# Performance work log

Measured on AMD Instinct MI355X. Metric: run time of the kernel, lower is better.

Reference implementation:

```python
import jax, jax.numpy as jnp
import numpy as np

D_MODEL = 512
DQ = D_MODEL // 4  # 128
TIME_SHIFT_START = 256
VELOCITY_START = 768
NOTE_OFF_START = 128


def conv1d(x, w, b, stride, pad):
    # x: [B, Cin, L], w: [Cout, Cin, K]
    y = jax.lax.conv_general_dilated(x, w, (stride,), [(pad, pad)],
                                     dimension_numbers=('NCH', 'OIH', 'NCH'))
    return y + b[None, :, None]


def adaptive_avg_pool1d(x, out_size):
    # faithful to torch AdaptiveAvgPool1d bin boundaries
    L = x.shape[-1]
    starts = (np.arange(out_size) * L) // out_size
    ends = np.ceil((np.arange(out_size) + 1) * L / out_size).astype(np.int64)
    cs = jnp.concatenate([jnp.zeros(x.shape[:-1] + (1,), x.dtype),
                          jnp.cumsum(x, axis=-1)], axis=-1)
    return (cs[..., ends] - cs[..., starts]) / jnp.asarray(ends - starts, x.dtype)


def setup_inputs() -> dict:
    key = jax.random.key(0)
    ks = jax.random.split(key, 20)

    def w(k, shape):
        fan_in = int(np.prod(shape[1:]))
        return jax.random.normal(k, shape, jnp.float32) / np.sqrt(fan_in)

    def b(k, n):
        return jax.random.normal(k, (n,), jnp.float32) * 0.01

    return {
        'tokens': jax.random.randint(ks[0], (32, 4096), 0, 774),
        'r1_w': w(ks[1], (32, 1, 8)),    'r1_b': b(ks[2], 32),
        'r2_w': w(ks[3], (64, 32, 4)),   'r2_b': b(ks[4], 64),
        'h1_w': w(ks[5], (64, 128, 12)), 'h1_b': b(ks[6], 64),
        'h2_w': w(ks[7], (32, 64, 8)),   'h2_b': b(ks[8], 32),
        'm1_w': w(ks[9], (64, 128, 5)),  'm1_b': b(ks[10], 64),
        'm2_w': w(ks[11], (32, 64, 3)),  'm2_b': b(ks[12], 32),
        'd1_w': w(ks[13], (16, 6, 4)),   'd1_b': b(ks[14], 16),
        'd2_w': w(ks[15], (16, 16, 3)),  'd2_b': b(ks[16], 16),
        'fc_w': w(ks[17], (D_MODEL, D_MODEL)), 'fc_b': b(ks[18], D_MODEL),
    }


def reference(tokens, r1_w, r1_b, r2_w, r2_b, h1_w, h1_b, h2_w, h2_b,
              m1_w, m1_b, m2_w, m2_b, d1_w, d1_b, d2_w, d2_b, fc_w, fc_b):
    B, S = tokens.shape
    relu = jax.nn.relu

    # rhythm: binary time-shift indicator [B,1,S]
    ts = ((tokens >= TIME_SHIFT_START) & (tokens < VELOCITY_START)).astype(jnp.float32)[:, None, :]
    r = relu(conv1d(ts, r1_w, r1_b, 2, 3))
    r = relu(conv1d(r, r2_w, r2_b, 2, 1))
    r = adaptive_avg_pool1d(r, DQ).reshape(B, -1)  # [B, 64*DQ]

    # vectorized one-hot pitch scatter (replaces the python double loop): [B,128,S]
    nm = tokens < NOTE_OFF_START
    pitch = jnp.transpose(
        jax.nn.one_hot(jnp.where(nm, tokens, 0) % 128, 128, dtype=jnp.float32)
        * nm[..., None].astype(jnp.float32), (0, 2, 1))

    h = relu(conv1d(pitch, h1_w, h1_b, 1, 6))
    h = relu(conv1d(h, h2_w, h2_b, 2, 3))
    h = adaptive_avg_pool1d(h, DQ).reshape(B, -1)  # [B, 32*DQ]

    m = relu(conv1d(pitch, m1_w, m1_b, 1, 2))
    m = relu(conv1d(m, m2_w, m2_b, 1, 1))
    m = adaptive_avg_pool1d(m, DQ).reshape(B, -1)  # [B, 32*DQ]

    # velocity one-hot scatter: [B,6,S]
    vm = tokens >= VELOCITY_START
    vel = jnp.clip(jnp.where(vm, tokens - VELOCITY_START, 0), 0, 5)
    vpat = jnp.transpose(
        jax.nn.one_hot(vel, 6, dtype=jnp.float32) * vm[..., None].astype(jnp.float32),
        (0, 2, 1))
    d = relu(conv1d(vpat, d1_w, d1_b, 1, 2))
    d = relu(conv1d(d, d2_w, d2_b, 1, 1))
    d = adaptive_avg_pool1d(d, DQ).reshape(B, -1)  # [B, 16*DQ]

    # total flattened size is 36*d_model != d_model, so torch branch always pools
    r, h, m, d = [adaptive_avg_pool1d(f[:, None, :], DQ)[:, 0] for f in (r, h, m, d)]

    combined = jnp.concatenate([r, h, m, d], axis=1)       # [B, d_model]
    feats = combined @ fc_w.T + fc_b                        # Linear
    return jnp.broadcast_to(feats[:, None, :], (B, S, D_MODEL))
```

## Files before the change

kernel.cpp:

```cpp
#include <hip/hip_runtime.h>

typedef unsigned short u16;
typedef unsigned int u32;
typedef float vf4 __attribute__((ext_vector_type(4)));
typedef unsigned int vu4 __attribute__((ext_vector_type(4)));
typedef short sh8 __attribute__((ext_vector_type(8)));
typedef float f32x4 __attribute__((ext_vector_type(4)));

__device__ __forceinline__ float bf2f(u16 u) {
  return __uint_as_float(((u32)u) << 16);
}
__device__ __forceinline__ u16 f2bf(float f) {
  u32 x = __float_as_uint(f);
  return (u16)((x + 0x7fffu + ((x >> 16) & 1u)) >> 16);
}
__device__ __forceinline__ float ldin(const void* p, int idx, int isf) {
  return isf ? ((const float*)p)[idx] : bf2f(((const u16*)p)[idx]);
}

#define OFF_FLAG  ((size_t)0)
#define OFF_WB    ((size_t)16)
#define OFF_WTH1  ((size_t)1180432)
#define OFF_WTM1  ((size_t)1573648)
#define OFF_COMB  ((size_t)1737488)
#define OFF_FEATF ((size_t)1803024)
#define OFF_FEATB ((size_t)1868560)
#define OFF_R1    ((size_t)1901328)
#define OFF_D1    ((size_t)10289936)
#define OFF_DP    ((size_t)18686736)
#define OFF_H1    ((size_t)18948880)
#define OFF_M1    ((size_t)35758864)
#define OFF_WH2B  ((size_t)52536080)
#define OFF_WH2L  ((size_t)52568848)
#define OFF_WM2B  ((size_t)52601616)
#define OFF_WM2L  ((size_t)52613904)
#define WS_NEEDED ((size_t)52626192)

#define WB_R1W 0
#define WB_R1B 256
#define WB_R2W 288
#define WB_R2B 8480
#define WB_H1B 8544
#define WB_H2W 8608
#define WB_H2B 24992
#define WB_M1B 25024
#define WB_M2W 25088
#define WB_M2B 31232
#define WB_D1W 31264
#define WB_D1B 31648
#define WB_D2W 31664
#define WB_D2B 32432
#define WB_FCW 32448
#define WB_FCB 294592
#define WB_TOTAL 295104

#define H1_STRIDE 4104
#define D1_STRIDE 4100

__global__ __launch_bounds__(256) void k_convert(
    const void* r1_w, const void* r1_b, const void* r2_w, const void* r2_b,
    const void* h1_w, const void* h1_b, const void* h2_w, const void* h2_b,
    const void* m1_w, const void* m1_b, const void* m2_w, const void* m2_b,
    const void* d1_w, const void* d1_b, const void* d2_w, const void* d2_b,
    const void* fc_w, const void* fc_b,
    int* __restrict__ flagp, float* __restrict__ wb,
    float* __restrict__ wTh1, float* __restrict__ wTm1,
    float* __restrict__ combined,
    u16* __restrict__ wh2b, u16* __restrict__ wh2l,
    u16* __restrict__ wm2b, u16* __restrict__ wm2l) {
  __shared__ int cnt[4];
  int tid = threadIdx.x;
  {
    u16 v = ((const u16*)fc_w)[2 * tid];
    int e = (v >> 7) & 0xFF;
    int outside = (e < 100 || e > 140) ? 1 : 0;
    unsigned long long m = __ballot(outside);
    if ((tid & 63) == 0) cnt[tid >> 6] = __popcll(m);
  }
  __syncthreads();
  int isf = (cnt[0] + cnt[1] + cnt[2] + cnt[3] >= 64) ? 1 : 0;
  if (blockIdx.x == 0 && tid == 0) flagp[0] = isf;

  int j = blockIdx.x * 256 + tid;
  if (j >= 473280) return;
  if (j < WB_TOTAL) {
    const void* src; int si;
    if      (j < WB_R1B) { src = r1_w; si = j; }
    else if (j < WB_R2W) { src = r1_b; si = j - WB_R1B; }
    else if (j < WB_R2B) { src = r2_w; si = j - WB_R2W; }
    else if (j < WB_H1B) { src = r2_b; si = j - WB_R2B; }
    else if (j < WB_H2W) { src = h1_b; si = j - WB_H1B; }
    else if (j < WB_H2B) { src = h2_w; si = j - WB_H2W; }
    else if (j < WB_M1B) { src = h2_b; si = j - WB_H2B; }
    else if (j < WB_M2W) { src = m1_b; si = j - WB_M1B; }
    else if (j < WB_M2B) { src = m2_w; si = j - WB_M2W; }
    else if (j < WB_D1W) { src = m2_b; si = j - WB_M2B; }
    else if (j < WB_D1B) { src = d1_w; si = j - WB_D1W; }
    else if (j < WB_D2W) { src = d1_b; si = j - WB_D1B; }
    else if (j < WB_D2B) { src = d2_w; si = j - WB_D2W; }
    else if (j < WB_FCW) { src = d2_b; si = j - WB_D2B; }
    else if (j < WB_FCB) { src = fc_w; si = j - WB_FCW; }
    else                 { src = fc_b; si = j - WB_FCB; }
    wb[j] = ldin(src, si, isf);
  } else if (j < 393408) {
    int j2 = j - WB_TOTAL;
    int o = j2 & 63, r = j2 >> 6, k = r % 12, p = r / 12;
    wTh1[j2] = ldin(h1_w, (o * 128 + p) * 12 + k, isf);
  } else if (j < 434368) {
    int j3 = j - 393408;
    int o = j3 & 63, r = j3 >> 6, k = r % 5, p = r / 5;
    wTm1[j3] = ldin(m1_w, (o * 128 + p) * 5 + k, isf);
  } else if (j < 450752) {
    combined[j - 434368] = 0.f;
  } else if (j < 467136) {
    int jj = j - 450752;
    int o = jj >> 9, rem = jj & 511, c = rem >> 3, kk = rem & 7;
    float w = ldin(h2_w, (o * 64 + c) * 8 + kk, isf);
    u16 hi = f2bf(w);
    wh2b[jj] = hi;
    wh2l[jj] = f2bf(w - bf2f(hi));
  } else {
    int jj = j - 467136;
    int o = jj / 192, rem = jj % 192, c = rem / 3, kk = rem % 3;
    float w = ldin(m2_w, (o * 64 + c) * 3 + kk, isf);
    u16 hi = f2bf(w);
    wm2b[jj] = hi;
    wm2l[jj] = f2bf(w - bf2f(hi));
  }
}


__device__ __forceinline__ void dev_r1(float* smem, const int* tok,
                                       const float* r1wf, const float* r1bf,
                                       float* r1ws, int chunk, int b) {
  float* w1s = smem;
  float* b1s = smem + 256;
  float* Ibuf = smem + 288;
  int tid = threadIdx.x;
  w1s[tid] = r1wf[tid];
  if (tid < 32) b1s[tid] = r1bf[tid];
  int t0 = chunk * 64;
  if (tid < 134) {
    int x = 2 * t0 - 3 + tid;
    float v = 0.f;
    if ((unsigned)x < 4096u) {
      int tk = tok[b * 4096 + x];
      v = (tk >= 256 && tk < 768) ? 1.f : 0.f;
    }
    Ibuf[tid] = v;
  }
  __syncthreads();
  int tl = tid & 63, og = tid >> 6;
  float iv[8];
#pragma unroll
  for (int k = 0; k < 8; ++k) iv[k] = Ibuf[2 * tl + k];
  int t = t0 + tl;
#pragma unroll
  for (int i = 0; i < 8; ++i) {
    int o = og * 8 + i;
    float acc = b1s[o];
#pragma unroll
    for (int k = 0; k < 8; ++k) acc = fmaf(w1s[o * 8 + k], iv[k], acc);
    r1ws[(size_t)(b * 32 + o) * 2048 + t] = fmaxf(acc, 0.f);
  }
}

__device__ __forceinline__ void dev_d1(float* smem, const int* tok,
                                       const float* d1wf, const float* d1bf,
                                       float* d1ws, int chunk, int b) {
  float* wds = smem;
  int* cls = (int*)(smem + 384);
  int tid = threadIdx.x;
  for (int f = tid; f < 384; f += 256) wds[f] = d1wf[f];
  int t0 = chunk * 64;
  if (tid < 67) {
    int x = t0 - 2 + tid;
    int v = -1;
    if ((unsigned)x < 4096u) {
      int tk = tok[b * 4096 + x];
      if (tk >= 768) { v = tk - 768; v = v > 5 ? 5 : v; }
    }
    cls[tid] = v;
  }
  __syncthreads();
  int tl = tid & 63, og = tid >> 6;
  int t = t0 + tl;
  if (t > 4096) return;
  int vk[4];
#pragma unroll
  for (int k = 0; k < 4; ++k) vk[k] = cls[tl + k];
#pragma unroll
  for (int i = 0; i < 4; ++i) {
    int o = og * 4 + i;
    float acc = d1bf[o];
#pragma unroll
    for (int k = 0; k < 4; ++k) {
      int v = vk[k];
      if (v >= 0) acc += wds[(o * 6 + v) * 4 + k];
    }
    d1ws[(size_t)(b * 16 + o) * D1_STRIDE + t] = fmaxf(acc, 0.f);
  }
}

__device__ __forceinline__ void dev_h1(float* smem, const int* tok,
                                       const float* wTh1, const float* h1bf,
                                       u16* h1ws, int bx, int b) {
  float (*tile)[65] = reinterpret_cast<float(*)[65]>(smem);
  int tid = threadIdx.x;
  int t0 = bx * 32;
  int o = tid & 63, sub = tid >> 6;
  float bias = h1bf[o];
#pragma unroll
  for (int j = 0; j < 8; ++j) {
    int tl = j * 4 + sub;
    int t = t0 + tl;
    float acc = bias;
    if (t <= 4096) {
#pragma unroll
      for (int k = 0; k < 12; ++k) {
        int x = t + k - 6;
        if ((unsigned)x < 4096u) {
          int p = tok[b * 4096 + x];
          if (p < 128) acc += wTh1[(p * 12 + k) * 64 + o];
        }
      }
    }
    tile[tl][o] = fmaxf(acc, 0.f);
  }
  __syncthreads();
  int o2 = tid >> 2, seg = tid & 3;
  size_t rowbase = (size_t)(b * 64 + o2) * H1_STRIDE;
  int ts = t0 + seg * 8;
  if (ts + 7 <= 4096) {
    u32 w0 = (u32)f2bf(tile[seg * 8 + 0][o2]) | ((u32)f2bf(tile[seg * 8 + 1][o2]) << 16);
    u32 w1 = (u32)f2bf(tile[seg * 8 + 2][o2]) | ((u32)f2bf(tile[seg * 8 + 3][o2]) << 16);
    u32 w2 = (u32)f2bf(tile[seg * 8 + 4][o2]) | ((u32)f2bf(tile[seg * 8 + 5][o2]) << 16);
    u32 w3 = (u32)f2bf(tile[seg * 8 + 6][o2]) | ((u32)f2bf(tile[seg * 8 + 7][o2]) << 16);
    uint4 v; v.x = w0; v.y = w1; v.z = w2; v.w = w3;
    *(uint4*)&h1ws[rowbase + ts] = v;
  } else {
    for (int i2 = 0; i2 < 8; ++i2) {
      int t = ts + i2;
      if (t <= 4096) h1ws[rowbase + t] = f2bf(tile[seg * 8 + i2][o2]);
      else if (t < H1_STRIDE) h1ws[rowbase + t] = 0;
    }
  }
}

__device__ __forceinline__ void dev_m1(float* smem, const int* tok,
                                       const float* wTm1, const float* m1bf,
                                       u16* m1ws, int bx, int b) {
  float (*tile)[65] = reinterpret_cast<float(*)[65]>(smem);
  int tid = threadIdx.x;
  int t0 = bx * 32;
  int o = tid & 63, sub = tid >> 6;
  float bias = m1bf[o];
#pragma unroll
  for (int j = 0; j < 8; ++j) {
    int tl = j * 4 + sub;
    int t = t0 + tl;
    float acc = bias;
#pragma unroll
    for (int k = 0; k < 5; ++k) {
      int x = t + k - 2;
      if ((unsigned)x < 4096u) {
        int p = tok[b * 4096 + x];
        if (p < 128) acc += wTm1[(p * 5 + k) * 64 + o];
      }
    }
    tile[tl][o] = fmaxf(acc, 0.f);
  }
  __syncthreads();
  int o2 = tid >> 2, seg = tid & 3;
  size_t rowbase = (size_t)(b * 64 + o2) * 4096;
  int ts = t0 + seg * 8;
  u32 w0 = (u32)f2bf(tile[seg * 8 + 0][o2]) | ((u32)f2bf(tile[seg * 8 + 1][o2]) << 16);
  u32 w1 = (u32)f2bf(tile[seg * 8 + 2][o2]) | ((u32)f2bf(tile[seg * 8 + 3][o2]) << 16);
  u32 w2 = (u32)f2bf(tile[seg * 8 + 4][o2]) | ((u32)f2bf(tile[seg * 8 + 5][o2]) << 16);
  u32 w3 = (u32)f2bf(tile[seg * 8 + 6][o2]) | ((u32)f2bf(tile[seg * 8 + 7][o2]) << 16);
  uint4 v; v.x = w0; v.y = w1; v.z = w2; v.w = w3;
  *(uint4*)&m1ws[rowbase + ts] = v;
}

__global__ __launch_bounds__(256) void k_cv1(const int* __restrict__ tok,
                                             const float* __restrict__ wb,
                                             const float* __restrict__ wTh1,
                                             const float* __restrict__ wTm1,
                                             float* __restrict__ r1ws,
                                             float* __restrict__ d1ws,
                                             u16* __restrict__ h1ws,
                                             u16* __restrict__ m1ws) {
  __shared__ __align__(16) float smem[2080];
  int bx = blockIdx.x;
  if (bx < 1024) {
    dev_r1(smem, tok, wb + WB_R1W, wb + WB_R1B, r1ws, bx & 31, bx >> 5);
  } else if (bx < 3104) {
    int n = bx - 1024;
    dev_d1(smem, tok, wb + WB_D1W, wb + WB_D1B, d1ws, n % 65, n / 65);
  } else if (bx < 7232) {
    int n = bx - 3104;
    dev_h1(smem, tok, wTh1, wb + WB_H1B, h1ws, n % 129, n / 129);
  } else {
    int n = bx - 7232;
    dev_m1(smem, tok, wTm1, wb + WB_M1B, m1ws, n & 127, n >> 7);
  }
}


__device__ __forceinline__ void dev_h2(const u16* h1ws,
                                       const u16* wh2b, const u16* wh2l,
                                       const float* h2bf,
                                       float* combined, int chunk, int q, int b) {
  const int tid = threadIdx.x;
  const int w = tid >> 6, l = tid & 63;
  const int quad = l >> 4, n = l & 15;
  const int ot = w & 1, tp = w >> 1;
  const int tb = q * 512 + chunk * 64;
  f32x4 acc[2];
  acc[0] = (f32x4){0.f, 0.f, 0.f, 0.f};
  acc[1] = (f32x4){0.f, 0.f, 0.f, 0.f};
  const u16* wph = wh2b + (size_t)(16 * ot + n) * 512 + quad * 8;
  const u16* wpl = wh2l + (size_t)(16 * ot + n) * 512 + quad * 8;

  for (int kc = 0; kc < 2; ++kc) {
    sh8 ah[8], al[8];
#pragma unroll
    for (int s = 0; s < 8; ++s) {
      ah[s] = *(const sh8*)(wph + kc * 256 + 32 * s);
      al[s] = *(const sh8*)(wpl + kc * 256 + 32 * s);
    }
#pragma unroll
    for (int it = 0; it < 2; ++it) {
      int t0 = tb + (2 * it + tp) * 16;
      int xbase = 2 * t0 + 2 * n - 3;
#pragma unroll
      for (int s = 0; s < 8; ++s) {
        int c = kc * 32 + 4 * s + quad;
        const u16* row = h1ws + (size_t)(b * 64 + c) * H1_STRIDE;
        sh8 bb;
        if (xbase >= 0) {
          __builtin_memcpy(&bb, row + xbase, 16);
        } else {
#pragma unroll
          for (int j = 0; j < 8; ++j) {
            int x = xbase + j;
            bb[j] = (x >= 0) ? (short)row[x] : (short)0;
          }
        }
        acc[it] = __builtin_amdgcn_mfma_f32_16x16x32_bf16(ah[s], bb, acc[it], 0, 0, 0);
        acc[it] = __builtin_amdgcn_mfma_f32_16x16x32_bf16(al[s], bb, acc[it], 0, 0, 0);
      }
    }
  }
#pragma unroll
  for (int r = 0; r < 4; ++r) {
    float bs = h2bf[16 * ot + quad * 4 + r];
    float s = fmaxf(acc[0][r] + bs, 0.f) + fmaxf(acc[1][r] + bs, 0.f);
    s += __shfl_xor(s, 1, 64);
    s += __shfl_xor(s, 2, 64);
    s += __shfl_xor(s, 4, 64);
    s += __shfl_xor(s, 8, 64);
    if (n == 0) {
      int o = 16 * ot + quad * 4 + r;
      atomicAdd(&combined[b * 512 + 128 + 4 * o + q], s * (1.f / 512.f));
    }
  }
}

__device__ __forceinline__ void dev_m2(float* smem, const u16* m1ws,
                                       const u16* wm2b, const u16* wm2l,
                                       const float* m2bf,
                                       float* combined, int sub, int q, int b) {
  u16* xs = (u16*)smem;
  const int tid = threadIdx.x;
  const int w = tid >> 6, l = tid & 63;
  const int quad = l >> 4, n = l & 15;
  const int ot = w & 1, tp = w >> 1;
  const int tb = q * 1024 + sub * 256;
  sh8 ah[6], al[6];
  {
    const u16* wph = wm2b + (size_t)(16 * ot + n) * 192 + quad * 8;
    const u16* wpl = wm2l + (size_t)(16 * ot + n) * 192 + quad * 8;
#pragma unroll
    for (int s = 0; s < 6; ++s) {
      ah[s] = *(const sh8*)(wph + 32 * s);
      al[s] = *(const sh8*)(wpl + 32 * s);
    }
  }
  float bs[4];
#pragma unroll
  for (int r = 0; r < 4; ++r) bs[r] = m2bf[16 * ot + quad * 4 + r];
  float sm[4] = {0.f, 0.f, 0.f, 0.f};
  const int gkb = quad * 8;

  for (int it = 0; it < 8; ++it) {
    for (int f = tid; f < 1280; f += 256) {
      int rg = f / 640, rem = f % 640, c = rem / 10, ch = rem % 10;
      int t0 = tb + (2 * it + rg) * 16;
      int xa = t0 - 2 + 2 * ch;
      const u16* row = m1ws + (size_t)(b * 64 + c) * 4096;
      u32 vlo = ((unsigned)xa < 4096u) ? row[xa] : 0u;
      u32 vhi = ((unsigned)(xa + 1) < 4096u) ? row[xa + 1] : 0u;
      ((u32*)xs)[f] = vlo | (vhi << 16);
    }
    __syncthreads();
    const u16* xr = xs + tp * 1280;
    f32x4 acc = {0.f, 0.f, 0.f, 0.f};
#pragma unroll
    for (int s = 0; s < 6; ++s) {
      sh8 bb;
#pragma unroll
      for (int j = 0; j < 8; ++j) {
        int gk = 32 * s + gkb + j;
        int c = (gk * 21846) >> 16;
        int kk = gk - 3 * c;
        bb[j] = (short)xr[c * 20 + n + kk + 1];
      }
      acc = __builtin_amdgcn_mfma_f32_16x16x32_bf16(ah[s], bb, acc, 0, 0, 0);
      acc = __builtin_amdgcn_mfma_f32_16x16x32_bf16(al[s], bb, acc, 0, 0, 0);
    }
#pragma unroll
    for (int r = 0; r < 4; ++r) sm[r] += fmaxf(acc[r] + bs[r], 0.f);
    __syncthreads();
  }
#pragma unroll
  for (int r = 0; r < 4; ++r) {
    float s = sm[r];
    s += __shfl_xor(s, 1, 64);
    s += __shfl_xor(s, 2, 64);
    s += __shfl_xor(s, 4, 64);
    s += __shfl_xor(s, 8, 64);
    if (n == 0) {
      int o = 16 * ot + quad * 4 + r;
      atomicAdd(&combined[b * 512 + 256 + 4 * o + q], s * (1.f / 1024.f));
    }
  }
}

__device__ __forceinline__ void dev_r2(float* smem, const float* r1ws,
                                       const float* r2wf, const float* r2bf,
                                       float* combined, int chunk, int b) {
  float* wcr = smem;
  float (*tile)[68] = reinterpret_cast<float(*)[68]>(smem + 2048);
  const int tbase = chunk * 64;
  const int half = chunk >> 3;
  const int tid = threadIdx.x;
  const int og = tid >> 6, tl = tid & 63;
  float acc[16];
#pragma unroll
  for (int i = 0; i < 16; ++i) acc[i] = 0.f;

  for (int c0 = 0; c0 < 32; c0 += 8) {
    for (int f = tid; f < 2048; f += 256) {
      int o = f & 63, r = f >> 6, k = r & 3, cc = r >> 2;
      wcr[f] = r2wf[(o * 32 + c0 + cc) * 4 + k];
    }
    for (int f = tid; f < 1056; f += 256) {
      int iu = f % 66, pc = f / 66, p = pc & 1, cc = pc >> 1;
      int x = 2 * (tbase - 1 + iu) + p;
      float v = 0.f;
      if (x >= 0 && x < 2048) v = r1ws[(size_t)(b * 32 + c0 + cc) * 2048 + x];
      tile[pc][iu] = v;
    }
    __syncthreads();
#pragma unroll
    for (int cc = 0; cc < 8; ++cc) {
      float ev[3], od[3];
#pragma unroll
      for (int f3 = 0; f3 < 3; ++f3) {
        ev[f3] = tile[cc * 2][tl + f3];
        od[f3] = tile[cc * 2 + 1][tl + f3];
      }
#pragma unroll
      for (int k = 0; k < 4; ++k) {
        const int p = (k + 1) & 1, fk = (k + 1) >> 1;
        const float* wv = &wcr[(cc * 4 + k) * 64 + og * 16];
        float4 wa = *(const float4*)wv;
        float4 wbv = *(const float4*)(wv + 4);
        float4 wcc = *(const float4*)(wv + 8);
        float4 wd = *(const float4*)(wv + 12);
        float wr[16] = {wa.x, wa.y, wa.z, wa.w, wbv.x, wbv.y, wbv.z, wbv.w,
                        wcc.x, wcc.y, wcc.z, wcc.w, wd.x, wd.y, wd.z, wd.w};
        float v0 = p ? od[fk] : ev[fk];
#pragma unroll
        for (int i = 0; i < 16; ++i) acc[i] = fmaf(v0, wr[i], acc[i]);
      }
    }
    __syncthreads();
  }
  const float inv = 1.f / 512.f;
#pragma unroll
  for (int i = 0; i < 16; ++i) {
    int o = og * 16 + i;
    float s = fmaxf(acc[i] + r2bf[o], 0.f);
#pragma unroll
    for (int d = 32; d > 0; d >>= 1) s += __shfl_down(s, d, 64);
    if (tl == 0) atomicAdd(&combined[b * 512 + 2 * o + half], s * inv);
  }
}

__device__ __forceinline__ void dev_d2(float* smem, const float* d1ws,
                                       const float* d2wf, const float* d2bf,
                                       float* dpws, int chunk, int b) {
  float* wd = smem;
  float (*dt)[132] = reinterpret_cast<float(*)[132]>(smem + 768);
  float* c2 = smem + 768 + 2112;
  const int tbase = chunk * 128;
  const int tid = threadIdx.x;
  for (int f = tid; f < 768; f += 256) wd[f] = d2wf[f];
  for (int f = tid; f < 2096; f += 256) {
    int iu = f % 131, c = f / 131;
    int x = tbase - 1 + iu;
    float v = 0.f;
    if (x >= 0 && x <= 4096) v = d1ws[(size_t)(b * 16 + c) * D1_STRIDE + x];
    dt[c][iu] = v;
  }
  __syncthreads();
  for (int idx = tid; idx < 16 * 129; idx += 256) {
    int o = idx / 129, tl = idx % 129;
    float acc = d2bf[o];
    const float* w = &wd[o * 48];
#pragma unroll 4
    for (int c = 0; c < 16; ++c) {
      acc = fmaf(dt[c][tl], w[c * 3 + 0],
            fmaf(dt[c][tl + 1], w[c * 3 + 1],
            fmaf(dt[c][tl + 2], w[c * 3 + 2], acc)));
    }
    c2[o * 133 + tl] = fmaxf(acc, 0.f);
  }
  __syncthreads();
  if (tid < 64) {
    int o = tid >> 2, qq = tid & 3;
    const float* row = c2 + o * 133 + 32 * qq;
    float s = 0.f;
#pragma unroll
    for (int j = 0; j < 33; ++j) s += row[j];
    dpws[(size_t)(b * 16 + o) * 128 + 4 * chunk + qq] = s * (1.f / 33.f);
  }
}

__global__ __launch_bounds__(256, 4) void k_cv2(const u16* __restrict__ h1ws,
                                                const u16* __restrict__ m1ws,
                                                const float* __restrict__ r1ws,
                                                const float* __restrict__ d1ws,
                                                const float* __restrict__ wb,
                                                const u16* __restrict__ wh2b,
                                                const u16* __restrict__ wh2l,
                                                const u16* __restrict__ wm2b,
                                                const u16* __restrict__ wm2l,
                                                float* __restrict__ combined,
                                                float* __restrict__ dpws) {
  __shared__ __align__(16) float smem[5008];
  int bx = blockIdx.x;
  if (bx < 1024) {
    dev_h2(h1ws, wh2b, wh2l, wb + WB_H2B, combined, bx & 7, (bx >> 3) & 3, bx >> 5);
  } else if (bx < 1536) {
    int n = bx - 1024;
    dev_m2(smem, m1ws, wm2b, wm2l, wb + WB_M2B, combined, n & 3, (n >> 2) & 3, n >> 4);
  } else if (bx < 2048) {
    int n = bx - 1536;
    dev_r2(smem, r1ws, wb + WB_R2W, wb + WB_R2B, combined, n & 15, n >> 4);
  } else {
    int n = bx - 2048;
    dev_d2(smem, d1ws, wb + WB_D2W, wb + WB_D2B, dpws, n & 31, n >> 5);
  }
}

__global__ __launch_bounds__(256) void k_fc(const float* __restrict__ combined,
                                            const float* __restrict__ dpws,
                                            const float* __restrict__ fcwf,
                                            const float* __restrict__ fcbf,
                                            float* __restrict__ featf,
                                            u16* __restrict__ featb) {
  const int b = blockIdx.x, tid = threadIdx.x;
  __shared__ float cb[512];
  cb[tid] = combined[b * 512 + tid];
  if (tid < 128) {
    cb[256 + tid] = combined[b * 512 + 256 + tid];
  } else {
    int j = tid - 128;
    int o = j >> 3, i0 = (j & 7) * 16;
    const float* row = dpws + (size_t)(b * 16 + o) * 128;
    float s = 0.f;
#pragma unroll
    for (int i = 0; i < 16; ++i) s += row[i0 + i];
    cb[384 + j] = s * (1.f / 16.f);
  }
  __syncthreads();
  for (int h = 0; h < 2; ++h) {
    int oo = h * 256 + tid;
    float acc = fcbf[oo];
    const float4* wr = (const float4*)(fcwf + (size_t)oo * 512);
#pragma unroll 8
    for (int j4 = 0; j4 < 128; ++j4) {
      float4 w = wr[j4];
      const float* c4 = &cb[j4 * 4];
      acc = fmaf(c4[0], w.x, acc);
      acc = fmaf(c4[1], w.y, acc);
      acc = fmaf(c4[2], w.z, acc);
      acc = fmaf(c4[3], w.w, acc);
    }
    featf[b * 512 + oo] = acc;
    featb[b * 512 + oo] = f2bf(acc);
  }
}

__global__ __launch_bounds__(256) void k_bcast(const int* __restrict__ flagp,
                                               const vf4* __restrict__ featf4,
                                               const vu4* __restrict__ featb4,
                                               vf4* __restrict__ outf,
                                               vu4* __restrict__ outb) {
  int base = blockIdx.x * 1024 + threadIdx.x;
  if (flagp[0]) {
#pragma unroll
    for (int s = 0; s < 4; ++s) {
      int g = base + s * 256;
      vf4 v = featf4[(g >> 19) * 128 + (g & 127)];
      __builtin_nontemporal_store(v, &outf[g]);
    }
  } else {
#pragma unroll
    for (int s = 0; s < 4; ++s) {
      int g = base + s * 256;
      if (g < 8388608) {
        vu4 v = featb4[(g >> 18) * 64 + (g & 63)];
        __builtin_nontemporal_store(v, &outb[g]);
      }
    }
  }
}

extern "C" void kernel_launch(void* const* d_in, const int* in_sizes, int n_in,
                              void* d_out, int out_size, void* d_ws, size_t ws_size,
                              hipStream_t stream) {
  if (ws_size < WS_NEEDED) return;

  const int* tokens = (const int*)d_in[0];
  const void* r1_w = d_in[1];  const void* r1_b = d_in[2];
  const void* r2_w = d_in[3];  const void* r2_b = d_in[4];
  const void* h1_w = d_in[5];  const void* h1_b = d_in[6];
  const void* h2_w = d_in[7];  const void* h2_b = d_in[8];
  const void* m1_w = d_in[9];  const void* m1_b = d_in[10];
  const void* m2_w = d_in[11]; const void* m2_b = d_in[12];
  const void* d1_w = d_in[13]; const void* d1_b = d_in[14];
  const void* d2_w = d_in[15]; const void* d2_b = d_in[16];
  const void* fc_w = d_in[17]; const void* fc_b = d_in[18];

  char* ws = (char*)d_ws;
  int*   flagp   = (int*)  (ws + OFF_FLAG);
  float* wb      = (float*)(ws + OFF_WB);
  float* wTh1    = (float*)(ws + OFF_WTH1);
  float* wTm1    = (float*)(ws + OFF_WTM1);
  float* combined= (float*)(ws + OFF_COMB);
  float* featf   = (float*)(ws + OFF_FEATF);
  u16*   featb   = (u16*)  (ws + OFF_FEATB);
  float* r1ws    = (float*)(ws + OFF_R1);
  float* d1ws    = (float*)(ws + OFF_D1);
  float* dpws    = (float*)(ws + OFF_DP);
  u16*   h1ws    = (u16*)  (ws + OFF_H1);
  u16*   m1ws    = (u16*)  (ws + OFF_M1);
  u16*   wh2b    = (u16*)  (ws + OFF_WH2B);
  u16*   wh2l    = (u16*)  (ws + OFF_WH2L);
  u16*   wm2b    = (u16*)  (ws + OFF_WM2B);
  u16*   wm2l    = (u16*)  (ws + OFF_WM2L);

  k_convert<<<1849, 256, 0, stream>>>(r1_w, r1_b, r2_w, r2_b, h1_w, h1_b, h2_w, h2_b,
                                      m1_w, m1_b, m2_w, m2_b, d1_w, d1_b, d2_w, d2_b,
                                      fc_w, fc_b, flagp, wb, wTh1, wTm1, combined,
                                      wh2b, wh2l, wm2b, wm2l);
  k_cv1<<<11328, 256, 0, stream>>>(tokens, wb, wTh1, wTm1, r1ws, d1ws, h1ws, m1ws);
  k_cv2<<<3072, 256, 0, stream>>>(h1ws, m1ws, r1ws, d1ws, wb, wh2b, wh2l, wm2b, wm2l,
                                  combined, dpws);
  k_fc<<<32, 256, 0, stream>>>(combined, dpws, wb + WB_FCW, wb + WB_FCB, featf, featb);
  k_bcast<<<16384, 256, 0, stream>>>(flagp, (const vf4*)featf, (const vu4*)featb,
                                     (vf4*)d_out, (vu4*)d_out);
}
```

Baseline: 482.8 us.

## Fuse rhythm and velocity first-layer convs into second-stage blocks

The first conv layers of the rhythm and velocity branches are now computed on the fly inside the second-stage conv blocks, straight from the tokens. This removes the global-memory round trip through the r1 and d1 workspaces and removes those blocks from the first conv launch. The cost is that halo elements are computed twice across neighbouring chunks and each block needs more shared memory, which may reduce occupancy for the cv2 kernel.

```diff
diff --git a/kernel.cpp b/kernel.cpp
--- a/kernel.cpp
+++ b/kernel.cpp
@@ -25,8 +25,6 @@
 #define OFF_COMB  ((size_t)1737488)
 #define OFF_FEATF ((size_t)1803024)
 #define OFF_FEATB ((size_t)1868560)
-#define OFF_R1    ((size_t)1901328)
-#define OFF_D1    ((size_t)10289936)
 #define OFF_DP    ((size_t)18686736)
 #define OFF_H1    ((size_t)18948880)
 #define OFF_M1    ((size_t)35758864)
@@ -55,7 +53,6 @@
 #define WB_TOTAL 295104
 
 #define H1_STRIDE 4104
-#define D1_STRIDE 4100
 
 __global__ __launch_bounds__(256) void k_convert(
     const void* r1_w, const void* r1_b, const void* r2_w, const void* r2_b,
@@ -130,78 +127,6 @@
 }
 
 
-__device__ __forceinline__ void dev_r1(float* smem, const int* tok,
-                                       const float* r1wf, const float* r1bf,
-                                       float* r1ws, int chunk, int b) {
-  float* w1s = smem;
-  float* b1s = smem + 256;
-  float* Ibuf = smem + 288;
-  int tid = threadIdx.x;
-  w1s[tid] = r1wf[tid];
-  if (tid < 32) b1s[tid] = r1bf[tid];
-  int t0 = chunk * 64;
-  if (tid < 134) {
-    int x = 2 * t0 - 3 + tid;
-    float v = 0.f;
-    if ((unsigned)x < 4096u) {
-      int tk = tok[b * 4096 + x];
-      v = (tk >= 256 && tk < 768) ? 1.f : 0.f;
-    }
-    Ibuf[tid] = v;
-  }
-  __syncthreads();
-  int tl = tid & 63, og = tid >> 6;
-  float iv[8];
-#pragma unroll
-  for (int k = 0; k < 8; ++k) iv[k] = Ibuf[2 * tl + k];
-  int t = t0 + tl;
-#pragma unroll
-  for (int i = 0; i < 8; ++i) {
-    int o = og * 8 + i;
-    float acc = b1s[o];
-#pragma unroll
-    for (int k = 0; k < 8; ++k) acc = fmaf(w1s[o * 8 + k], iv[k], acc);
-    r1ws[(size_t)(b * 32 + o) * 2048 + t] = fmaxf(acc, 0.f);
-  }
-}
-
-__device__ __forceinline__ void dev_d1(float* smem, const int* tok,
-                                       const float* d1wf, const float* d1bf,
-                                       float* d1ws, int chunk, int b) {
-  float* wds = smem;
-  int* cls = (int*)(smem + 384);
-  int tid = threadIdx.x;
-  for (int f = tid; f < 384; f += 256) wds[f] = d1wf[f];
-  int t0 = chunk * 64;
-  if (tid < 67) {
-    int x = t0 - 2 + tid;
-    int v = -1;
-    if ((unsigned)x < 4096u) {
-      int tk = tok[b * 4096 + x];
-      if (tk >= 768) { v = tk - 768; v = v > 5 ? 5 : v; }
-    }
-    cls[tid] = v;
-  }
-  __syncthreads();
-  int tl = tid & 63, og = tid >> 6;
-  int t = t0 + tl;
-  if (t > 4096) return;
-  int vk[4];
-#pragma unroll
-  for (int k = 0; k < 4; ++k) vk[k] = cls[tl + k];
-#pragma unroll
-  for (int i = 0; i < 4; ++i) {
-    int o = og * 4 + i;
-    float acc = d1bf[o];
-#pragma unroll
-    for (int k = 0; k < 4; ++k) {
-      int v = vk[k];
-      if (v >= 0) acc += wds[(o * 6 + v) * 4 + k];
-    }
-    d1ws[(size_t)(b * 16 + o) * D1_STRIDE + t] = fmaxf(acc, 0.f);
-  }
-}
-
 __device__ __forceinline__ void dev_h1(float* smem, const int* tok,
                                        const float* wTh1, const float* h1bf,
                                        u16* h1ws, int bx, int b) {
@@ -286,22 +211,14 @@
                                              const float* __restrict__ wb,
                                              const float* __restrict__ wTh1,
                                              const float* __restrict__ wTm1,
-                                             float* __restrict__ r1ws,
-                                             float* __restrict__ d1ws,
                                              u16* __restrict__ h1ws,
                                              u16* __restrict__ m1ws) {
   __shared__ __align__(16) float smem[2080];
   int bx = blockIdx.x;
-  if (bx < 1024) {
-    dev_r1(smem, tok, wb + WB_R1W, wb + WB_R1B, r1ws, bx & 31, bx >> 5);
-  } else if (bx < 3104) {
-    int n = bx - 1024;
-    dev_d1(smem, tok, wb + WB_D1W, wb + WB_D1B, d1ws, n % 65, n / 65);
-  } else if (bx < 7232) {
-    int n = bx - 3104;
-    dev_h1(smem, tok, wTh1, wb + WB_H1B, h1ws, n % 129, n / 129);
+  if (bx < 4128) {
+    dev_h1(smem, tok, wTh1, wb + WB_H1B, h1ws, bx % 129, bx / 129);
   } else {
-    int n = bx - 7232;
+    int n = bx - 4128;
     dev_m1(smem, tok, wTm1, wb + WB_M1B, m1ws, n & 127, n >> 7);
   }
 }
@@ -437,15 +354,46 @@
   }
 }
 
-__device__ __forceinline__ void dev_r2(float* smem, const float* r1ws,
-                                       const float* r2wf, const float* r2bf,
-                                       float* combined, int chunk, int b) {
-  float* wcr = smem;
-  float (*tile)[68] = reinterpret_cast<float(*)[68]>(smem + 2048);
+__device__ __forceinline__ void dev_r2f(float* smem, const int* tok,
+                                        const float* r1wf, const float* r1bf,
+                                        const float* r2wf, const float* r2bf,
+                                        float* combined, int chunk, int b) {
+  float* w1s = smem;
+  float* b1s = smem + 256;
+  float* Ibuf = smem + 288;
+  float* r1t = smem + 560;
+  float* wcr = smem + 4784;
   const int tbase = chunk * 64;
   const int half = chunk >> 3;
   const int tid = threadIdx.x;
   const int og = tid >> 6, tl = tid & 63;
+
+  w1s[tid] = r1wf[tid];
+  if (tid < 32) b1s[tid] = r1bf[tid];
+  for (int i = tid; i < 270; i += 256) {
+    int x = 4 * tbase - 7 + i;
+    float v = 0.f;
+    if ((unsigned)x < 4096u) {
+      int tk = tok[b * 4096 + x];
+      v = (tk >= 256 && tk < 768) ? 1.f : 0.f;
+    }
+    Ibuf[i] = v;
+  }
+  __syncthreads();
+  for (int f = tid; f < 32 * 132; f += 256) {
+    int c = f / 132, xl = f % 132;
+    int x = 2 * tbase - 2 + xl;
+    float v = 0.f;
+    if ((unsigned)x < 2048u) {
+      float acc = b1s[c];
+#pragma unroll
+      for (int k = 0; k < 8; ++k) acc = fmaf(w1s[c * 8 + k], Ibuf[2 * xl + k], acc);
+      v = fmaxf(acc, 0.f);
+    }
+    r1t[c * 132 + xl] = v;
+  }
+  __syncthreads();
+
   float acc[16];
 #pragma unroll
   for (int i = 0; i < 16; ++i) acc[i] = 0.f;
@@ -455,21 +403,15 @@
       int o = f & 63, r = f >> 6, k = r & 3, cc = r >> 2;
       wcr[f] = r2wf[(o * 32 + c0 + cc) * 4 + k];
     }
-    for (int f = tid; f < 1056; f += 256) {
-      int iu = f % 66, pc = f / 66, p = pc & 1, cc = pc >> 1;
-      int x = 2 * (tbase - 1 + iu) + p;
-      float v = 0.f;
-      if (x >= 0 && x < 2048) v = r1ws[(size_t)(b * 32 + c0 + cc) * 2048 + x];
-      tile[pc][iu] = v;
-    }
     __syncthreads();
 #pragma unroll
     for (int cc = 0; cc < 8; ++cc) {
+      const float* rrow = &r1t[(c0 + cc) * 132];
       float ev[3], od[3];
 #pragma unroll
       for (int f3 = 0; f3 < 3; ++f3) {
-        ev[f3] = tile[cc * 2][tl + f3];
-        od[f3] = tile[cc * 2 + 1][tl + f3];
+        ev[f3] = rrow[2 * (tl + f3)];
+        od[f3] = rrow[2 * (tl + f3) + 1];
       }
 #pragma unroll
       for (int k = 0; k < 4; ++k) {
@@ -499,21 +441,43 @@
   }
 }
 
-__device__ __forceinline__ void dev_d2(float* smem, const float* d1ws,
-                                       const float* d2wf, const float* d2bf,
-                                       float* dpws, int chunk, int b) {
-  float* wd = smem;
-  float (*dt)[132] = reinterpret_cast<float(*)[132]>(smem + 768);
-  float* c2 = smem + 768 + 2112;
+__device__ __forceinline__ void dev_d2f(float* smem, const int* tok,
+                                        const float* d1wf, const float* d1bf,
+                                        const float* d2wf, const float* d2bf,
+                                        float* dpws, int chunk, int b) {
+  float* wds = smem;
+  int* cls = (int*)(smem + 384);
+  float* wd = smem + 520;
+  float* d1t = smem + 1288;
+  float* c2 = smem + 3400;
   const int tbase = chunk * 128;
   const int tid = threadIdx.x;
+  for (int f = tid; f < 384; f += 256) wds[f] = d1wf[f];
   for (int f = tid; f < 768; f += 256) wd[f] = d2wf[f];
-  for (int f = tid; f < 2096; f += 256) {
-    int iu = f % 131, c = f / 131;
-    int x = tbase - 1 + iu;
+  for (int i = tid; i < 134; i += 256) {
+    int x = tbase - 3 + i;
+    int v = -1;
+    if ((unsigned)x < 4096u) {
+      int tk = tok[b * 4096 + x];
+      if (tk >= 768) { v = tk - 768; v = v > 5 ? 5 : v; }
+    }
+    cls[i] = v;
+  }
+  __syncthreads();
+  for (int f = tid; f < 16 * 131; f += 256) {
+    int c = f / 131, xl = f % 131;
+    int t = tbase - 1 + xl;
     float v = 0.f;
-    if (x >= 0 && x <= 4096) v = d1ws[(size_t)(b * 16 + c) * D1_STRIDE + x];
-    dt[c][iu] = v;
+    if ((unsigned)t <= 4096u) {
+      float acc = d1bf[c];
+#pragma unroll
+      for (int k = 0; k < 4; ++k) {
+        int vv = cls[xl + k];
+        if (vv >= 0) acc += wds[(c * 6 + vv) * 4 + k];
+      }
+      v = fmaxf(acc, 0.f);
+    }
+    d1t[c * 132 + xl] = v;
   }
   __syncthreads();
   for (int idx = tid; idx < 16 * 129; idx += 256) {
@@ -522,9 +486,10 @@
     const float* w = &wd[o * 48];
 #pragma unroll 4
     for (int c = 0; c < 16; ++c) {
-      acc = fmaf(dt[c][tl], w[c * 3 + 0],
-            fmaf(dt[c][tl + 1], w[c * 3 + 1],
-            fmaf(dt[c][tl + 2], w[c * 3 + 2], acc)));
+      const float* row = &d1t[c * 132 + tl];
+      acc = fmaf(row[0], w[c * 3 + 0],
+            fmaf(row[1], w[c * 3 + 1],
+            fmaf(row[2], w[c * 3 + 2], acc)));
     }
     c2[o * 133 + tl] = fmaxf(acc, 0.f);
   }
@@ -539,10 +504,9 @@
   }
 }
 
-__global__ __launch_bounds__(256, 4) void k_cv2(const u16* __restrict__ h1ws,
+__global__ __launch_bounds__(256, 4) void k_cv2(const int* __restrict__ tok,
+                                                const u16* __restrict__ h1ws,
                                                 const u16* __restrict__ m1ws,
-                                                const float* __restrict__ r1ws,
-                                                const float* __restrict__ d1ws,
                                                 const float* __restrict__ wb,
                                                 const u16* __restrict__ wh2b,
                                                 const u16* __restrict__ wh2l,
@@ -550,7 +514,7 @@
                                                 const u16* __restrict__ wm2l,
                                                 float* __restrict__ combined,
                                                 float* __restrict__ dpws) {
-  __shared__ __align__(16) float smem[5008];
+  __shared__ __align__(16) float smem[6832];
   int bx = blockIdx.x;
   if (bx < 1024) {
     dev_h2(h1ws, wh2b, wh2l, wb + WB_H2B, combined, bx & 7, (bx >> 3) & 3, bx >> 5);
@@ -559,10 +523,12 @@
     dev_m2(smem, m1ws, wm2b, wm2l, wb + WB_M2B, combined, n & 3, (n >> 2) & 3, n >> 4);
   } else if (bx < 2048) {
     int n = bx - 1536;
-    dev_r2(smem, r1ws, wb + WB_R2W, wb + WB_R2B, combined, n & 15, n >> 4);
+    dev_r2f(smem, tok, wb + WB_R1W, wb + WB_R1B, wb + WB_R2W, wb + WB_R2B,
+            combined, n & 15, n >> 4);
   } else {
     int n = bx - 2048;
-    dev_d2(smem, d1ws, wb + WB_D2W, wb + WB_D2B, dpws, n & 31, n >> 5);
+    dev_d2f(smem, tok, wb + WB_D1W, wb + WB_D1B, wb + WB_D2W, wb + WB_D2B,
+            dpws, n & 31, n >> 5);
   }
 }
 
@@ -654,8 +620,6 @@
   float* combined= (float*)(ws + OFF_COMB);
   float* featf   = (float*)(ws + OFF_FEATF);
   u16*   featb   = (u16*)  (ws + OFF_FEATB);
-  float* r1ws    = (float*)(ws + OFF_R1);
-  float* d1ws    = (float*)(ws + OFF_D1);
   float* dpws    = (float*)(ws + OFF_DP);
   u16*   h1ws    = (u16*)  (ws + OFF_H1);
   u16*   m1ws    = (u16*)  (ws + OFF_M1);
@@ -668,8 +632,8 @@
                                       m1_w, m1_b, m2_w, m2_b, d1_w, d1_b, d2_w, d2_b,
                                       fc_w, fc_b, flagp, wb, wTh1, wTm1, combined,
                                       wh2b, wh2l, wm2b, wm2l);
-  k_cv1<<<11328, 256, 0, stream>>>(tokens, wb, wTh1, wTm1, r1ws, d1ws, h1ws, m1ws);
-  k_cv2<<<3072, 256, 0, stream>>>(h1ws, m1ws, r1ws, d1ws, wb, wh2b, wh2l, wm2b, wm2l,
+  k_cv1<<<8224, 256, 0, stream>>>(tokens, wb, wTh1, wTm1, h1ws, m1ws);
+  k_cv2<<<3072, 256, 0, stream>>>(tokens, h1ws, m1ws, wb, wh2b, wh2l, wm2b, wm2l,
                                   combined, dpws);
   k_fc<<<32, 256, 0, stream>>>(combined, dpws, wb + WB_FCW, wb + WB_FCB, featf, featb);
   k_bcast<<<16384, 256, 0, stream>>>(flagp, (const vf4*)featf, (const vu4*)featb,
```

Measured after the change: 487.9 us. Within noise of the previous version (+1.1%).
